# Optimization experiments

Hardware: AMD Instinct MI355X
Metric: run time of the kernel (lower is better)

## Reference

```python
import jax, jax.numpy as jnp
import numpy as np

D_MODEL = 1024
N_HEADS = 16
D_HEAD = D_MODEL // N_HEADS


def setup_inputs() -> dict:
    key = jax.random.key(0)
    kx, kq, kk, kv = jax.random.split(key, 4)
    B, T = 2, 2048
    X = jax.random.normal(kx, (B, T, D_MODEL), dtype=jnp.float32)
    s = 1.0 / np.sqrt(D_MODEL)
    # torch nn.Linear weight is [out, in]; y = x @ W.T
    Wq = jax.random.uniform(kq, (D_MODEL, D_MODEL), jnp.float32, -s, s)
    Wk = jax.random.uniform(kk, (D_MODEL, D_MODEL), jnp.float32, -s, s)
    Wv = jax.random.uniform(kv, (D_MODEL, D_MODEL), jnp.float32, -s, s)
    return {"X": X, "Wq": Wq, "Wk": Wk, "Wv": Wv}


def reference(X, Wq, Wk, Wv):
    B, T, _ = X.shape
    def heads(W):
        # x @ W.T -> [B,T,D] -> [B,H,T,Dh]
        return (X @ W.T).reshape(B, T, N_HEADS, D_HEAD).transpose(0, 2, 1, 3)
    Q, K, V = heads(Wq), heads(Wk), heads(Wv)
    scores = jnp.einsum('bhqd,bhkd->bhqk', Q, K)
    causal = jnp.tril(jnp.ones((T, T), dtype=bool))
    # original masks with -inf BEFORE scaling; -inf/scale == -inf, so equivalent
    scores = jnp.where(causal, scores, -jnp.inf) / jnp.sqrt(jnp.float32(D_HEAD))
    attn = jax.nn.softmax(scores, axis=-1)
    out = jnp.einsum('bhqk,bhkd->bhqd', attn, V)
    return out.transpose(0, 2, 1, 3).reshape(B, T, N_HEADS * D_HEAD)
```

## Files before the change

### kernel.cpp

```cpp
#include <hip/hip_runtime.h>


using bf16x8  = __attribute__((ext_vector_type(8))) __bf16;
using floatx4 = __attribute__((ext_vector_type(4))) float;

#define T_SEQ   2048
#define D_MODEL 1024
#define N_HEADS 16
#define D_HEAD  64
#define BATCH   2
#define M_TOT   4096
#define N_TOT   3072
#define PLANE   (T_SEQ * D_HEAD)
#define NX      (M_TOT * D_MODEL)
#define NWSEG   (D_MODEL * D_MODEL)
#define QSCALE  0.18033688f
#define SM_BIAS 24.0f

__device__ __forceinline__ unsigned short f32_to_bf16(float f) {
  unsigned int u = __float_as_uint(f);
  u += 0x7fffu + ((u >> 16) & 1u);
  return (unsigned short)(u >> 16);
}
__device__ __forceinline__ unsigned int pack2_bf16(float a, float b) {
  unsigned int ua = __float_as_uint(a) + 0x8000u;
  unsigned int ub = __float_as_uint(b) + 0x8000u;
  return __builtin_amdgcn_perm(ub, ua, 0x07060302);
}
__device__ __forceinline__ void async_cp16(void* lds, const void* gptr) {
  __builtin_amdgcn_global_load_lds(
      (const __attribute__((address_space(1))) unsigned int*)gptr,
      (__attribute__((address_space(3))) unsigned int*)lds, 16, 0, 0);
}

__global__ __launch_bounds__(256) void cvt_kernel(
    const float* __restrict__ X,  const float* __restrict__ Wq,
    const float* __restrict__ Wk, const float* __restrict__ Wv,
    unsigned short* __restrict__ Xb, unsigned short* __restrict__ Wb)
{
  const size_t i = ((size_t)blockIdx.x * 256 + threadIdx.x) * 8;
  const float* src;
  unsigned short* dst;
  if (i < NX) { src = X + i; dst = Xb + i; }
  else {
    const size_t r = i - NX;
    const int w = (int)(r >> 20);
    const size_t o = r & (NWSEG - 1);
    src = ((w == 0) ? Wq : (w == 1) ? Wk : Wv) + o;
    dst = Wb + r;
  }
  float4 f0 = *(const float4*)src;
  float4 f1 = *(const float4*)(src + 4);
  uint4 out;
  out.x = pack2_bf16(f0.x, f0.y);
  out.y = pack2_bf16(f0.z, f0.w);
  out.z = pack2_bf16(f1.x, f1.y);
  out.w = pack2_bf16(f1.z, f1.w);
  *(uint4*)dst = out;
}

__global__ __launch_bounds__(256) void gemm_qkv(
    const unsigned short* __restrict__ Xb,
    const unsigned short* __restrict__ Wb,
    unsigned short* __restrict__ Qb,
    unsigned short* __restrict__ Kb,
    unsigned short* __restrict__ VTb)
{
  __shared__ unsigned short Als[128 * 64];
  __shared__ unsigned short Bls[128 * 64];

  const int tid  = threadIdx.x;
  const int lane = tid & 63;
  const int wave = tid >> 6;
  const int l15  = lane & 15;
  const int quad = lane >> 4;
  const int wm   = wave >> 1, wn = wave & 1;

  const int n_blk = blockIdx.x * 128;
  const int m_blk = blockIdx.y * 128;

  const int swz = (((tid >> 3) ^ tid) & 7) * 8;
  const unsigned short* Ag = Xb + (size_t)(m_blk + (tid >> 3)) * D_MODEL + swz;
  const unsigned short* Bg = Wb + (size_t)(n_blk + (tid >> 3)) * D_MODEL + swz;
  char* Alds = (char*)Als + wave * 1024;
  char* Blds = (char*)Bls + wave * 1024;

  floatx4 acc[4][4] = {};

  for (int k0 = 0; k0 < D_MODEL; k0 += 64) {
    __syncthreads();
#pragma unroll
    for (int p = 0; p < 4; p++) {
      async_cp16(Alds + p * 4096, Ag + (size_t)p * 32 * D_MODEL + k0);
      async_cp16(Blds + p * 4096, Bg + (size_t)p * 32 * D_MODEL + k0);
    }
    __syncthreads();

#pragma unroll
    for (int ks = 0; ks < 2; ks++) {
      bf16x8 a[4], b[4];
#pragma unroll
      for (int i = 0; i < 4; i++) {
        const int sa = ((ks * 4 + quad) ^ (l15 & 7)) * 16;
        a[i] = *(const bf16x8*)((char*)Als + (wm * 64 + 16 * i + l15) * 128 + sa);
        b[i] = *(const bf16x8*)((char*)Bls + (wn * 64 + 16 * i + l15) * 128 + sa);
      }
#pragma unroll
      for (int mi = 0; mi < 4; mi++)
#pragma unroll
        for (int ni = 0; ni < 4; ni++)
          acc[mi][ni] = __builtin_amdgcn_mfma_f32_16x16x32_bf16(a[mi], b[ni], acc[mi][ni], 0, 0, 0);
    }
  }

  __syncthreads();
  char* ep = (char*)Als + wave * 8192;
  const int w_sel  = n_blk >> 10;
  const int m_base = m_blk + wm * 64;
  const int n_base = n_blk + wn * 64;
  const int h      = (n_base & 1023) >> 6;
  const float csc  = (w_sel == 0) ? QSCALE : 1.0f;

  if (w_sel < 2) {
#pragma unroll
    for (int mi = 0; mi < 4; mi++)
#pragma unroll
      for (int ni = 0; ni < 4; ni++)
#pragma unroll
        for (int r = 0; r < 4; r++) {
          const int row  = 16 * mi + quad * 4 + r;
          const int colb = (16 * ni + l15) * 2;
          const int phys = ((colb >> 4) ^ (row & 7)) * 16;
          *(unsigned short*)(ep + row * 128 + phys + (colb & 15)) =
              f32_to_bf16(acc[mi][ni][r] * csc);
        }
  } else {
#pragma unroll
    for (int mi = 0; mi < 4; mi++)
#pragma unroll
      for (int ni = 0; ni < 4; ni++)
#pragma unroll
        for (int r = 0; r < 4; r++) {
          const int row  = 16 * ni + l15;
          const int colb = (16 * mi + quad * 4 + r) * 2;
          const int phys = ((colb >> 4) ^ (row & 7)) * 16;
          *(unsigned short*)(ep + row * 128 + phys + (colb & 15)) =
              f32_to_bf16(acc[mi][ni][r]);
        }
  }
  asm volatile("s_waitcnt lgkmcnt(0)" ::: "memory");

#pragma unroll
  for (int pass = 0; pass < 8; pass++) {
    const int row  = pass * 8 + (lane >> 3);
    const int phys = ((lane & 7) ^ (row & 7)) * 16;
    uint4 v = *(const uint4*)(ep + row * 128 + phys);
    if (w_sel < 2) {
      const int m  = m_base + row;
      const int bb = m >> 11;
      const int t  = m & (T_SEQ - 1);
      unsigned short* dst = ((w_sel == 0) ? Qb : Kb) +
          ((size_t)(bb * N_HEADS + h) * T_SEQ + t) * D_HEAD + (lane & 7) * 8;
      *(uint4*)dst = v;
    } else {
      const int bb = m_base >> 11;
      unsigned short* dst = VTb +
          ((size_t)(bb * N_HEADS + h) * D_HEAD + row) * T_SEQ + (m_base & (T_SEQ - 1)) + (lane & 7) * 8;
      *(uint4*)dst = v;
    }
  }
}

__global__ __launch_bounds__(256) void attn_kernel(
    const unsigned short* __restrict__ Qb,
    const unsigned short* __restrict__ Kb,
    const unsigned short* __restrict__ VTb,
    float* __restrict__ Out)
{
  __shared__ unsigned short Ks[2][64 * 64];
  __shared__ unsigned short Vs[2][64 * 64];
  __shared__ unsigned short Ps[4][16 * 64];

  const int tid  = threadIdx.x;
  const int lane = tid & 63;
  const int wave = tid >> 6;
  const int l15  = lane & 15;
  const int quad = lane >> 4;

  const int bh   = blockIdx.x & 31;
  const int pair = blockIdx.x >> 5;

  const unsigned short* Qp = Qb  + (size_t)bh * PLANE;
  const unsigned short* Kp = Kb  + (size_t)bh * PLANE;
  const unsigned short* Vp = VTb + (size_t)bh * PLANE;

  const int swz = (((tid >> 3) ^ tid) & 7) * 8;
  const unsigned short* Kg = Kp + (size_t)(tid >> 3) * D_HEAD + swz;
  const unsigned short* Vg = Vp + (size_t)(tid >> 3) * T_SEQ + swz;
  char* myp = (char*)Ps[wave];
  const int b = bh >> 4, h = bh & 15;

#pragma unroll 1
  for (int it = 0; it < 2; it++) {
    const int strip = it ? (31 - pair) : pair;
    const int q0w   = strip * 64 + wave * 16;
    const int nch   = strip + 1;

    bf16x8 aq[2];
#pragma unroll
    for (int s = 0; s < 2; s++)
      aq[s] = *(const bf16x8*)(Qp + (size_t)(q0w + l15) * D_HEAD + 32 * s + quad * 8);

    float l_lane = 0.0f;
    floatx4 o[4] = {};

    __syncthreads();

#pragma unroll
    for (int p = 0; p < 2; p++) {
      async_cp16((char*)Ks[0] + p * 4096 + wave * 1024, Kg + (size_t)(p * 32) * D_HEAD);
      async_cp16((char*)Vs[0] + p * 4096 + wave * 1024, Vg + (size_t)(p * 32) * T_SEQ);
    }

    for (int jc = 0; jc < nch; jc++) {
      __syncthreads();
      if (jc + 1 < nch) {
        const int j1 = (jc + 1) * 64;
        char* kd = (char*)Ks[(jc + 1) & 1];
        char* vd = (char*)Vs[(jc + 1) & 1];
#pragma unroll
        for (int p = 0; p < 2; p++) {
          async_cp16(kd + p * 4096 + wave * 1024, Kg + (size_t)(j1 + p * 32) * D_HEAD);
          async_cp16(vd + p * 4096 + wave * 1024, Vg + (size_t)(p * 32) * T_SEQ + j1);
        }
      }
      const char* Ksb = (const char*)Ks[jc & 1];
      const char* Vsb = (const char*)Vs[jc & 1];

      floatx4 s[4] = {};
#pragma unroll
      for (int t = 0; t < 4; t++)
#pragma unroll
        for (int ss = 0; ss < 2; ss++) {
          const int sa = ((ss * 4 + quad) ^ (l15 & 7)) * 16;
          bf16x8 bk = *(const bf16x8*)(Ksb + (16 * t + l15) * 128 + sa);
          s[t] = __builtin_amdgcn_mfma_f32_16x16x32_bf16(bk, aq[ss], s[t], 0, 0, 0);
        }

      if (jc == nch - 1) {
        const int j0 = jc * 64;
        const int q  = q0w + l15;
#pragma unroll
        for (int t = 0; t < 4; t++) {
          const int kb = j0 + 16 * t + quad * 4;
#pragma unroll
          for (int r = 0; r < 4; r++)
            if (kb + r > q) s[t][r] = -INFINITY;
        }
      }

#pragma unroll
      for (int t = 0; t < 4; t++)
#pragma unroll
        for (int r = 0; r < 4; r++)
          s[t][r] = __builtin_amdgcn_exp2f(s[t][r] - SM_BIAS);
#pragma unroll
      for (int t = 0; t < 4; t++)
        l_lane += (s[t][0] + s[t][1]) + (s[t][2] + s[t][3]);

#pragma unroll
      for (int t = 0; t < 4; t++) {
        uint2 w;
        asm("v_cvt_pk_bf16_f32 %0, %1, %2" : "=v"(w.x) : "v"(s[t][0]), "v"(s[t][1]));
        asm("v_cvt_pk_bf16_f32 %0, %1, %2" : "=v"(w.y) : "v"(s[t][2]), "v"(s[t][3]));
        const int phys = (((2 * t + (quad >> 1)) ^ (l15 & 7)) * 16) + 8 * (quad & 1);
        *(uint2*)(myp + l15 * 128 + phys) = w;
      }
      asm volatile("s_waitcnt lgkmcnt(0)" ::: "memory");

#pragma unroll
      for (int ks = 0; ks < 2; ks++) {
        const int pa = ((ks * 4 + quad) ^ (l15 & 7)) * 16;
        bf16x8 ap = *(const bf16x8*)(myp + l15 * 128 + pa);
#pragma unroll
        for (int n = 0; n < 4; n++) {
          const int sa = ((ks * 4 + quad) ^ (l15 & 7)) * 16;
          bf16x8 bv = *(const bf16x8*)(Vsb + (16 * n + l15) * 128 + sa);
          o[n] = __builtin_amdgcn_mfma_f32_16x16x32_bf16(ap, bv, o[n], 0, 0, 0);
        }
      }
    }

    l_lane += __shfl_xor(l_lane, 16);
    l_lane += __shfl_xor(l_lane, 32);

#pragma unroll
    for (int r = 0; r < 4; r++) {
      const float inv_l = 1.0f / __shfl(l_lane, quad * 4 + r);
      const int t = q0w + quad * 4 + r;
#pragma unroll
      for (int n = 0; n < 4; n++)
        Out[(size_t)(b * T_SEQ + t) * D_MODEL + h * D_HEAD + 16 * n + l15] = o[n][r] * inv_l;
    }
  }
}

extern "C" void kernel_launch(void* const* d_in, const int* in_sizes, int n_in,
                              void* d_out, int out_size, void* d_ws, size_t ws_size,
                              hipStream_t stream) {
  const float* X  = (const float*)d_in[0];
  const float* Wq = (const float*)d_in[1];
  const float* Wk = (const float*)d_in[2];
  const float* Wv = (const float*)d_in[3];

  unsigned short* Qb = (unsigned short*)d_ws;
  unsigned short* Kb = Qb + (size_t)BATCH * N_HEADS * T_SEQ * D_HEAD;
  unsigned short* VT = Kb + (size_t)BATCH * N_HEADS * T_SEQ * D_HEAD;

  unsigned short* Xb = (unsigned short*)d_out;
  unsigned short* Wb = Xb + (size_t)NX;

  cvt_kernel<<<3584, 256, 0, stream>>>(X, Wq, Wk, Wv, Xb, Wb);

  dim3 g1(N_TOT / 128, M_TOT / 128);
  gemm_qkv<<<g1, 256, 0, stream>>>(Xb, Wb, Qb, Kb, VT);

  attn_kernel<<<512, 256, 0, stream>>>(Qb, Kb, VT, (float*)d_out);
}
```

Measured before the change: 152.4 us.

## Switch attention to 32x32x16 MFMA with 2x2 q/k wave split and register-resident P

The attention kernel now splits each 64x64 tile across waves as 2 query halves by 2 key halves and uses 32x32x16 bf16 MFMAs instead of 16x16x32. The P matrix is rearranged in registers with v_permlane32_swap rather than being round-tripped through per-wave LDS, which removes the LDS store, waitcnt and reload. Waves whose key half lies fully above the causal diagonal skip their work. Because each key-half wave holds a partial output, the two partial O and row sums are reduced through LDS in an epilogue that also writes coalesced float4 stores. The extra barriers and the reduction add overhead, and the causal skip leaves some waves idle on diagonal tiles.

New measurement: 154.5 us. About the same (+1.3%).

```diff
diff --git a/kernel.cpp b/kernel.cpp
--- a/kernel.cpp
+++ b/kernel.cpp
@@ -1,8 +1,10 @@
 #include <hip/hip_runtime.h>
 
 
-using bf16x8  = __attribute__((ext_vector_type(8))) __bf16;
-using floatx4 = __attribute__((ext_vector_type(4))) float;
+using bf16x8   = __attribute__((ext_vector_type(8))) __bf16;
+using floatx4  = __attribute__((ext_vector_type(4))) float;
+using floatx16 = __attribute__((ext_vector_type(16))) float;
+using uintx4   = __attribute__((ext_vector_type(4))) unsigned int;
 
 #define T_SEQ   2048
 #define D_MODEL 1024
@@ -177,15 +179,15 @@
     const unsigned short* __restrict__ VTb,
     float* __restrict__ Out)
 {
-  __shared__ unsigned short Ks[2][64 * 64];
-  __shared__ unsigned short Vs[2][64 * 64];
-  __shared__ unsigned short Ps[4][16 * 64];
+  __shared__ __align__(16) char smem[34304];
 
   const int tid  = threadIdx.x;
   const int lane = tid & 63;
   const int wave = tid >> 6;
-  const int l15  = lane & 15;
-  const int quad = lane >> 4;
+  const int l31  = lane & 31;
+  const int q1   = lane >> 5;
+  const int wq   = wave & 1;
+  const int wk   = wave >> 1;
 
   const int bh   = blockIdx.x & 31;
   const int pair = blockIdx.x >> 5;
@@ -197,111 +199,138 @@
   const int swz = (((tid >> 3) ^ tid) & 7) * 8;
   const unsigned short* Kg = Kp + (size_t)(tid >> 3) * D_HEAD + swz;
   const unsigned short* Vg = Vp + (size_t)(tid >> 3) * T_SEQ + swz;
-  char* myp = (char*)Ps[wave];
   const int b = bh >> 4, h = bh & 15;
+
+  char* const Ks0 = smem;
+  char* const Ks1 = smem + 8192;
+  char* const Vs0 = smem + 16384;
+  char* const Vs1 = smem + 24576;
+  float* const LB = (float*)(smem + 33792);
 
 #pragma unroll 1
   for (int it = 0; it < 2; it++) {
     const int strip = it ? (31 - pair) : pair;
-    const int q0w   = strip * 64 + wave * 16;
+    const int qbase = strip * 64 + wq * 32;
     const int nch   = strip + 1;
 
-    bf16x8 aq[2];
-#pragma unroll
-    for (int s = 0; s < 2; s++)
-      aq[s] = *(const bf16x8*)(Qp + (size_t)(q0w + l15) * D_HEAD + 32 * s + quad * 8);
-
-    float l_lane = 0.0f;
-    floatx4 o[4] = {};
+    bf16x8 aq[4];
+#pragma unroll
+    for (int kp = 0; kp < 4; kp++)
+      aq[kp] = *(const bf16x8*)(Qp + (size_t)(qbase + l31) * D_HEAD + kp * 16 + q1 * 8);
+
+    floatx16 o0 = {}, o1 = {};
+    float l_acc = 0.0f;
 
     __syncthreads();
 
 #pragma unroll
     for (int p = 0; p < 2; p++) {
-      async_cp16((char*)Ks[0] + p * 4096 + wave * 1024, Kg + (size_t)(p * 32) * D_HEAD);
-      async_cp16((char*)Vs[0] + p * 4096 + wave * 1024, Vg + (size_t)(p * 32) * T_SEQ);
+      async_cp16(Ks0 + p * 4096 + wave * 1024, Kg + (size_t)(p * 32) * D_HEAD);
+      async_cp16(Vs0 + p * 4096 + wave * 1024, Vg + (size_t)(p * 32) * T_SEQ);
     }
 
     for (int jc = 0; jc < nch; jc++) {
       __syncthreads();
       if (jc + 1 < nch) {
         const int j1 = (jc + 1) * 64;
-        char* kd = (char*)Ks[(jc + 1) & 1];
-        char* vd = (char*)Vs[(jc + 1) & 1];
+        char* kd = ((jc + 1) & 1) ? Ks1 : Ks0;
+        char* vd = ((jc + 1) & 1) ? Vs1 : Vs0;
 #pragma unroll
         for (int p = 0; p < 2; p++) {
           async_cp16(kd + p * 4096 + wave * 1024, Kg + (size_t)(j1 + p * 32) * D_HEAD);
           async_cp16(vd + p * 4096 + wave * 1024, Vg + (size_t)(p * 32) * T_SEQ + j1);
         }
       }
-      const char* Ksb = (const char*)Ks[jc & 1];
-      const char* Vsb = (const char*)Vs[jc & 1];
-
-      floatx4 s[4] = {};
-#pragma unroll
-      for (int t = 0; t < 4; t++)
-#pragma unroll
-        for (int ss = 0; ss < 2; ss++) {
-          const int sa = ((ss * 4 + quad) ^ (l15 & 7)) * 16;
-          bf16x8 bk = *(const bf16x8*)(Ksb + (16 * t + l15) * 128 + sa);
-          s[t] = __builtin_amdgcn_mfma_f32_16x16x32_bf16(bk, aq[ss], s[t], 0, 0, 0);
-        }
-
-      if (jc == nch - 1) {
-        const int j0 = jc * 64;
-        const int q  = q0w + l15;
-#pragma unroll
-        for (int t = 0; t < 4; t++) {
-          const int kb = j0 + 16 * t + quad * 4;
-#pragma unroll
-          for (int r = 0; r < 4; r++)
-            if (kb + r > q) s[t][r] = -INFINITY;
+      const char* Ksb = (jc & 1) ? Ks1 : Ks0;
+      const char* Vsb = (jc & 1) ? Vs1 : Vs0;
+      const int kbase = jc * 64 + wk * 32;
+
+      if (kbase <= qbase + 31) {
+        floatx16 s = {};
+        const int krow = wk * 32 + l31;
+#pragma unroll
+        for (int kp = 0; kp < 4; kp++) {
+          const int phys = (((2 * kp + q1) ^ (krow & 7)) * 16);
+          bf16x8 ak = *(const bf16x8*)(Ksb + krow * 128 + phys);
+          s = __builtin_amdgcn_mfma_f32_32x32x16_bf16(ak, aq[kp], s, 0, 0, 0);
+        }
+
+        if (kbase >= qbase) {
+          const int q = qbase + l31;
+#pragma unroll
+          for (int r = 0; r < 16; r++) {
+            const int kk = kbase + (r & 3) + 8 * (r >> 2) + 4 * q1;
+            if (kk > q) s[r] = -INFINITY;
+          }
+        }
+
+        float pv[16];
+#pragma unroll
+        for (int r = 0; r < 16; r++)
+          pv[r] = __builtin_amdgcn_exp2f(s[r] - SM_BIAS);
+#pragma unroll
+        for (int r = 0; r < 16; r += 4)
+          l_acc += (pv[r] + pv[r + 1]) + (pv[r + 2] + pv[r + 3]);
+
+        unsigned int w[8];
+#pragma unroll
+        for (int m = 0; m < 8; m++)
+          asm("v_cvt_pk_bf16_f32 %0, %1, %2" : "=v"(w[m]) : "v"(pv[2 * m]), "v"(pv[2 * m + 1]));
+
+#pragma unroll
+        for (int kp = 0; kp < 2; kp++) {
+          unsigned int b0 = w[4 * kp],     b2 = w[4 * kp + 2];
+          unsigned int b1 = w[4 * kp + 1], b3 = w[4 * kp + 3];
+          asm("v_permlane32_swap_b32 %0, %1" : "+v"(b0), "+v"(b2));
+          asm("v_permlane32_swap_b32 %0, %1" : "+v"(b1), "+v"(b3));
+          uintx4 u; u[0] = b0; u[1] = b1; u[2] = b2; u[3] = b3;
+          const bf16x8 pf = __builtin_bit_cast(bf16x8, u);
+
+          const int c = 4 * wk + 2 * kp + q1;
+          const int row0 = l31;
+          bf16x8 av0 = *(const bf16x8*)(Vsb + row0 * 128 + ((c ^ (row0 & 7)) * 16));
+          o0 = __builtin_amdgcn_mfma_f32_32x32x16_bf16(av0, pf, o0, 0, 0, 0);
+          const int row1 = 32 + l31;
+          bf16x8 av1 = *(const bf16x8*)(Vsb + row1 * 128 + ((c ^ (row1 & 7)) * 16));
+          o1 = __builtin_amdgcn_mfma_f32_32x32x16_bf16(av1, pf, o1, 0, 0, 0);
         }
       }
-
-#pragma unroll
-      for (int t = 0; t < 4; t++)
-#pragma unroll
-        for (int r = 0; r < 4; r++)
-          s[t][r] = __builtin_amdgcn_exp2f(s[t][r] - SM_BIAS);
-#pragma unroll
-      for (int t = 0; t < 4; t++)
-        l_lane += (s[t][0] + s[t][1]) + (s[t][2] + s[t][3]);
-
-#pragma unroll
-      for (int t = 0; t < 4; t++) {
-        uint2 w;
-        asm("v_cvt_pk_bf16_f32 %0, %1, %2" : "=v"(w.x) : "v"(s[t][0]), "v"(s[t][1]));
-        asm("v_cvt_pk_bf16_f32 %0, %1, %2" : "=v"(w.y) : "v"(s[t][2]), "v"(s[t][3]));
-        const int phys = (((2 * t + (quad >> 1)) ^ (l15 & 7)) * 16) + 8 * (quad & 1);
-        *(uint2*)(myp + l15 * 128 + phys) = w;
-      }
-      asm volatile("s_waitcnt lgkmcnt(0)" ::: "memory");
-
-#pragma unroll
-      for (int ks = 0; ks < 2; ks++) {
-        const int pa = ((ks * 4 + quad) ^ (l15 & 7)) * 16;
-        bf16x8 ap = *(const bf16x8*)(myp + l15 * 128 + pa);
-#pragma unroll
-        for (int n = 0; n < 4; n++) {
-          const int sa = ((ks * 4 + quad) ^ (l15 & 7)) * 16;
-          bf16x8 bv = *(const bf16x8*)(Vsb + (16 * n + l15) * 128 + sa);
-          o[n] = __builtin_amdgcn_mfma_f32_16x16x32_bf16(ap, bv, o[n], 0, 0, 0);
-        }
-      }
-    }
-
-    l_lane += __shfl_xor(l_lane, 16);
-    l_lane += __shfl_xor(l_lane, 32);
-
-#pragma unroll
-    for (int r = 0; r < 4; r++) {
-      const float inv_l = 1.0f / __shfl(l_lane, quad * 4 + r);
-      const int t = q0w + quad * 4 + r;
-#pragma unroll
-      for (int n = 0; n < 4; n++)
-        Out[(size_t)(b * T_SEQ + t) * D_MODEL + h * D_HEAD + 16 * n + l15] = o[n][r] * inv_l;
-    }
+    }
+
+    float la = l_acc, lb = l_acc;
+    asm("v_permlane32_swap_b32 %0, %1" : "+v"(la), "+v"(lb));
+    const float lt = la + lb;
+
+    __syncthreads();
+
+    float* ob = (float*)smem + (wk * 2 + wq) * (64 * 33);
+#pragma unroll
+    for (int r = 0; r < 16; r++) {
+      const int d0 = (r & 3) + 8 * (r >> 2) + 4 * q1;
+      ob[d0 * 33 + l31]        = o0[r];
+      ob[(32 + d0) * 33 + l31] = o1[r];
+    }
+    if (lane < 32) LB[wk * 64 + wq * 32 + l31] = lt;
+    __syncthreads();
+
+    const int row = tid >> 2;
+    const int dg  = tid & 3;
+    const int wqr = row >> 5, ql = row & 31;
+    const float inv = 1.0f / (LB[row] + LB[64 + row]);
+    const float* obA = (const float*)smem + (0 * 2 + wqr) * (64 * 33);
+    const float* obB = (const float*)smem + (1 * 2 + wqr) * (64 * 33);
+
+    float vout[16];
+#pragma unroll
+    for (int i = 0; i < 16; i++) {
+      const int d = dg * 16 + i;
+      vout[i] = (obA[d * 33 + ql] + obB[d * 33 + ql]) * inv;
+    }
+    const int t = strip * 64 + row;
+    float* dst = Out + (size_t)(b * T_SEQ + t) * D_MODEL + h * D_HEAD + dg * 16;
+#pragma unroll
+    for (int m = 0; m < 4; m++)
+      *(float4*)(dst + 4 * m) = *(const float4*)(vout + 4 * m);
   }
 }
 
```
